# Optimization experiments

Measured on AMD Instinct MI355X. Metric: run time of the kernel, lower is better.

The kernel has to match this reference:

```python
import jax, jax.numpy as jnp
import numpy as np
import math

HEADS = 8
DIM_HEAD = 64


def setup_inputs() -> dict:
    key = jax.random.key(0)
    k1, k2, k3 = jax.random.split(key, 3)
    b, n, dim = 4, 2048, 512
    inner = HEADS * DIM_HEAD  # 512
    x = jax.random.normal(k1, (b, n, dim), dtype=jnp.float32)
    W_qkv = jax.random.normal(k2, (dim, 4 * inner), dtype=jnp.float32) * (dim ** -0.5)
    W_out = jax.random.normal(k3, (2 * inner, dim), dtype=jnp.float32) * ((2 * inner) ** -0.5)
    b_out = jnp.zeros((dim,), dtype=jnp.float32)
    return {"x": x, "W_qkv": W_qkv, "W_out": W_out, "b_out": b_out}


def reference(x, W_qkv, W_out, b_out):
    b, n, d = x.shape
    h, dh = HEADS, DIM_HEAD
    scale = dh ** -0.5
    qkvt = x @ W_qkv  # [b, n, 4*h*dh]
    q, k, v, t = jnp.split(qkvt, 4, axis=-1)
    # 'b n (h d) -> b h n d'
    def to_heads(z):
        return z.reshape(b, n, h, dh).transpose(0, 2, 1, 3)
    q, k, v, t = map(to_heads, (q, k, v, t))

    # Branch 1: standard softmax attention
    dots = jnp.einsum('bhid,bhjd->bhij', q, k) * scale
    attn1 = jax.nn.softmax(dots, axis=-1)
    out1 = jnp.einsum('bhij,bhjd->bhid', attn1, v)

    # Branch 2: fixed positional-decay attention (shared across b, h; no repeat needed)
    pos = jnp.arange(1, n + 1, dtype=x.dtype)  # linspace(1, n, n)
    tg = jnp.abs(pos[None, :] - pos[:, None])  # |j - i|, [n, n]
    attn2 = jnp.exp(-tg / jnp.asarray(math.e, dtype=x.dtype))
    # NOTE: original divides by sum(-1) WITHOUT keepdim -> broadcasts over columns:
    # attn2[i, j] / sum_k attn2[j, k]
    attn2 = attn2 / attn2.sum(-1)
    out2 = jnp.einsum('ij,bhjd->bhid', attn2, t)

    out = jnp.concatenate([out1, out2], axis=-1)  # [b, h, n, 2*dh]
    out = out.transpose(0, 2, 1, 3).reshape(b, n, 2 * h * dh)  # 'b h n d -> b n (h d)'
    return out @ W_out + b_out
```

## Files before the change

kernel.cpp:

```cpp
#include <hip/hip_runtime.h>
#include <hip/hip_bf16.h>

#define B_ 4
#define N_ 2048
#define D_ 512
#define H_ 8
#define DH_ 64

typedef float float4_ __attribute__((ext_vector_type(4)));
typedef int int2_ __attribute__((ext_vector_type(2)));
typedef int int4_ __attribute__((ext_vector_type(4)));
typedef unsigned short ushort4_ __attribute__((ext_vector_type(4)));
typedef unsigned short ushort8_ __attribute__((ext_vector_type(8)));
typedef __bf16 bf16x8 __attribute__((ext_vector_type(8)));
typedef _Float16 half2_ __attribute__((ext_vector_type(2)));
typedef _Float16 half4_ __attribute__((ext_vector_type(4)));
typedef _Float16 half8_ __attribute__((ext_vector_type(8)));

#if __has_builtin(__builtin_amdgcn_exp2f)
#define EXP2(x) __builtin_amdgcn_exp2f(x)
#else
#define EXP2(x) exp2f(x)
#endif

__device__ __forceinline__ float b2f(unsigned short u) {
  union { unsigned int u; float f; } v; v.u = ((unsigned int)u) << 16; return v.f;
}
__device__ __forceinline__ unsigned short f2b(float f) {
  union { float f; unsigned int u; } v; v.f = f;
  unsigned int r = v.u + 0x7fffu + ((v.u >> 16) & 1u);
  return (unsigned short)(r >> 16);
}
__device__ __forceinline__ half4_ pk4(float a, float b, float c, float d) {
  half2_ lo = __builtin_bit_cast(half2_, __builtin_amdgcn_cvt_pkrtz(a, b));
  half2_ hi = __builtin_bit_cast(half2_, __builtin_amdgcn_cvt_pkrtz(c, d));
  return __builtin_bit_cast(half4_,
      (int2_){__builtin_bit_cast(int, lo), __builtin_bit_cast(int, hi)});
}
__device__ __forceinline__ half8_ cat44(half4_ a, half4_ b) {
  int2_ ia = __builtin_bit_cast(int2_, a), ib = __builtin_bit_cast(int2_, b);
  int4_ r = {ia[0], ia[1], ib[0], ib[1]};
  return __builtin_bit_cast(half8_, r);
}

#define GLD16(gp, lp)                                                        \
  __builtin_amdgcn_global_load_lds(                                          \
      (const __attribute__((address_space(1))) unsigned int*)(gp),           \
      (__attribute__((address_space(3))) unsigned int*)(lp), 16, 0, 0)

#define VMCNT(n) asm volatile("s_waitcnt vmcnt(" #n ")" ::: "memory")
#define SCHED0   __builtin_amdgcn_sched_barrier(0)
#define SBAR     __builtin_amdgcn_s_barrier()

__device__ __forceinline__ bool detect_fp32_local(
    const unsigned short* __restrict__ xhdr, int* cnt_sh) {
  if (threadIdx.x == 0) *cnt_sh = 0;
  __syncthreads();
  unsigned int e = (xhdr[threadIdx.x] >> 7) & 0xFFu;
  if (e >= 134u) atomicAdd(cnt_sh, 1);
  __syncthreads();
  return *cnt_sh > 16;
}

__device__ __forceinline__ void transpose_conv(
    const void* __restrict__ src, unsigned short* __restrict__ dst,
    int R, int C, int bx, int by, bool ofp) {
  __shared__ unsigned short tile[32][33];
  const int c0 = bx * 32, r0 = by * 32;
  const int tx = threadIdx.x & 31, ty = threadIdx.x >> 5;
#pragma unroll
  for (int k = 0; k < 4; ++k) {
    int r = ty + k * 8;
    long idx = (long)(r0 + r) * C + c0 + tx;
    tile[r][tx] = ofp ? f2b(((const float*)src)[idx])
                      : ((const unsigned short*)src)[idx];
  }
  __syncthreads();
#pragma unroll
  for (int k = 0; k < 4; ++k) {
    int c = ty + k * 8;
    dst[(long)(c0 + c) * R + r0 + tx] = tile[tx][c];
  }
}

__global__ __launch_bounds__(256) void prep_all(
    const void* __restrict__ xraw, const void* __restrict__ Wqraw,
    const void* __restrict__ Woraw, unsigned short* __restrict__ xb,
    unsigned short* __restrict__ WqT, unsigned short* __restrict__ WoT,
    unsigned short* __restrict__ Wband) {
  __shared__ int cnt_sh;
  const bool ofp = detect_fp32_local((const unsigned short*)xraw, &cnt_sh);
  const int bid = blockIdx.x;
  if (bid < 4096) {
    int i4 = bid * 256 + threadIdx.x;
    ushort4_ o;
    if (ofp) {
      float4_ v = ((const float4_*)xraw)[i4];
      o[0] = f2b(v[0]); o[1] = f2b(v[1]); o[2] = f2b(v[2]); o[3] = f2b(v[3]);
    } else {
      o = ((const ushort4_*)xraw)[i4];
    }
    *(ushort4_*)(xb + (long)i4 * 4) = o;
  } else if (bid < 5120) {
    const int b2 = bid - 4096;
    transpose_conv(Wqraw, WqT, 512, 2048, b2 % 64, b2 / 64, ofp);
  } else if (bid < 5632) {
    const int b2 = bid - 5120;
    transpose_conv(Woraw, WoT, 1024, 512, b2 % 16, b2 / 16, ofp);
  } else {
    constexpr float INV_E = 0.36787944117144233f;
    constexpr float R1 = 0.69220062755534635f;
    constexpr float INV_1MR = 3.2488706f;
    const int i = bid - 5632;
    const int krel = threadIdx.x;
    const int j = (i >> 6) * 64 - 96 + krel;
    float c = 0.f;
    if (j >= 0 && j < N_) {
      float wgt = __expf(-fabsf((float)(i - j)) * INV_E);
      float rj = __expf(-(float)j * INV_E);
      float rnj = __expf(-(float)(N_ - 1 - j) * INV_E);
      float S = 1.f + R1 * (2.f - rj - rnj) * INV_1MR;
      c = wgt / S;
    }
    _Float16 hv = (_Float16)c;
    Wband[i * 256 + krel] = __builtin_bit_cast(unsigned short, hv);
  }
}

#define MFMA16x32(d, a, b) \
  d = __builtin_amdgcn_mfma_f32_16x16x32_bf16(a, b, d, 0, 0, 0)

__global__ __launch_bounds__(512, 2) void gemm256(
    const unsigned short* __restrict__ A, const unsigned short* __restrict__ Bt,
    unsigned short* __restrict__ C, int M, int N, int K) {
  __shared__ unsigned short As[2][16384];
  __shared__ unsigned short Bs[2][16384];
  const int tid = threadIdx.x;
  const int w = tid >> 6, lane = tid & 63, l16 = lane & 15, quad = lane >> 4;
  const int wm = w >> 2, wn = w & 3;
  const int flat = blockIdx.x + blockIdx.y * 32;
  const int xc = flat & 7, jj = flat >> 3;
  const int bx = xc * 4 + (jj & 3), by = jj >> 2;
  const long tm = (long)bx * 256, tn = (long)by * 256;

  const int srow = tid >> 3;
  const int sch = (tid & 7) ^ (srow & 7);
  const unsigned short* gA = A + (tm + srow) * (long)K + sch * 8;
  const unsigned short* gB = Bt + (tn + srow) * (long)K + sch * 8;

  const int xr8 = l16 & 7;
  const int ch0 = ((0 + quad) ^ xr8) * 8;
  const int ch1 = ((4 + quad) ^ xr8) * 8;
  const int rowA0 = (wm * 128 + l16) * 64;
  const int rowB0 = (wn * 64 + l16) * 64;

  float4_ acc[8][4] = {};

  auto stage = [&](int t, int bufn) __attribute__((always_inline)) {
#pragma unroll
    for (int r = 0; r < 4; ++r)
      GLD16(gA + (long)(r * 64) * K + t * 64, &As[bufn][r * 4096 + w * 512]);
#pragma unroll
    for (int r = 0; r < 4; ++r)
      GLD16(gB + (long)(r * 64) * K + t * 64, &Bs[bufn][r * 4096 + w * 512]);
  };

  stage(0, 0);
  asm volatile("s_waitcnt vmcnt(0)" ::: "memory");
  __builtin_amdgcn_s_barrier();

  const int NT = K >> 6;
  for (int t = 0; t < NT; ++t) {
    const int buf = t & 1;
    const unsigned short* as = As[buf];
    const unsigned short* bs = Bs[buf];
    bf16x8 af[8], bq[4], br[4];
#pragma unroll
    for (int mi = 0; mi < 4; ++mi) {
      af[mi * 2]     = __builtin_bit_cast(bf16x8, *(const int4_*)&as[rowA0 + mi * 1024 + ch0]);
      af[mi * 2 + 1] = __builtin_bit_cast(bf16x8, *(const int4_*)&as[rowA0 + mi * 1024 + ch1]);
    }
#pragma unroll
    for (int ni = 0; ni < 2; ++ni) {
      bq[ni * 2]     = __builtin_bit_cast(bf16x8, *(const int4_*)&bs[rowB0 + ni * 1024 + ch0]);
      bq[ni * 2 + 1] = __builtin_bit_cast(bf16x8, *(const int4_*)&bs[rowB0 + ni * 1024 + ch1]);
    }
    if (t + 1 < NT) stage(t + 1, buf ^ 1);
    __builtin_amdgcn_s_barrier();
    asm volatile("s_waitcnt lgkmcnt(0)" ::: "memory");
    __builtin_amdgcn_sched_barrier(0);
    __builtin_amdgcn_s_setprio(1);
#pragma unroll
    for (int mi = 0; mi < 4; ++mi)
#pragma unroll
      for (int ni = 0; ni < 2; ++ni) {
        MFMA16x32(acc[mi][ni], af[mi * 2], bq[ni * 2]);
        MFMA16x32(acc[mi][ni], af[mi * 2 + 1], bq[ni * 2 + 1]);
      }
    __builtin_amdgcn_s_setprio(0);
    __builtin_amdgcn_s_barrier();
#pragma unroll
    for (int ni = 0; ni < 2; ++ni) {
      br[ni * 2]     = __builtin_bit_cast(bf16x8, *(const int4_*)&bs[rowB0 + (2 + ni) * 1024 + ch0]);
      br[ni * 2 + 1] = __builtin_bit_cast(bf16x8, *(const int4_*)&bs[rowB0 + (2 + ni) * 1024 + ch1]);
    }
    __builtin_amdgcn_s_barrier();
    asm volatile("s_waitcnt lgkmcnt(0)" ::: "memory");
    __builtin_amdgcn_sched_barrier(0);
    __builtin_amdgcn_s_setprio(1);
#pragma unroll
    for (int mi = 0; mi < 4; ++mi)
#pragma unroll
      for (int ni = 0; ni < 2; ++ni) {
        MFMA16x32(acc[mi][2 + ni], af[mi * 2], br[ni * 2]);
        MFMA16x32(acc[mi][2 + ni], af[mi * 2 + 1], br[ni * 2 + 1]);
      }
    __builtin_amdgcn_s_setprio(0);
    __builtin_amdgcn_s_barrier();
#pragma unroll
    for (int mi = 0; mi < 4; ++mi) {
      af[mi * 2]     = __builtin_bit_cast(bf16x8, *(const int4_*)&as[rowA0 + (4 + mi) * 1024 + ch0]);
      af[mi * 2 + 1] = __builtin_bit_cast(bf16x8, *(const int4_*)&as[rowA0 + (4 + mi) * 1024 + ch1]);
    }
    __builtin_amdgcn_s_barrier();
    asm volatile("s_waitcnt lgkmcnt(0)" ::: "memory");
    __builtin_amdgcn_sched_barrier(0);
    __builtin_amdgcn_s_setprio(1);
#pragma unroll
    for (int mi = 0; mi < 4; ++mi)
#pragma unroll
      for (int ni = 0; ni < 2; ++ni) {
        MFMA16x32(acc[4 + mi][2 + ni], af[mi * 2], br[ni * 2]);
        MFMA16x32(acc[4 + mi][2 + ni], af[mi * 2 + 1], br[ni * 2 + 1]);
      }
    __builtin_amdgcn_s_setprio(0);
    __builtin_amdgcn_s_barrier();
#pragma unroll
    for (int ni = 0; ni < 2; ++ni) {
      bq[ni * 2]     = __builtin_bit_cast(bf16x8, *(const int4_*)&bs[rowB0 + ni * 1024 + ch0]);
      bq[ni * 2 + 1] = __builtin_bit_cast(bf16x8, *(const int4_*)&bs[rowB0 + ni * 1024 + ch1]);
    }
    __builtin_amdgcn_s_barrier();
    asm volatile("s_waitcnt lgkmcnt(0)" ::: "memory");
    __builtin_amdgcn_sched_barrier(0);
    __builtin_amdgcn_s_setprio(1);
#pragma unroll
    for (int mi = 0; mi < 4; ++mi)
#pragma unroll
      for (int ni = 0; ni < 2; ++ni) {
        MFMA16x32(acc[4 + mi][ni], af[mi * 2], bq[ni * 2]);
        MFMA16x32(acc[4 + mi][ni], af[mi * 2 + 1], bq[ni * 2 + 1]);
      }
    __builtin_amdgcn_s_setprio(0);
    asm volatile("s_waitcnt vmcnt(0)" ::: "memory");
    __builtin_amdgcn_sched_barrier(0);
    __builtin_amdgcn_s_barrier();
  }
#pragma unroll
  for (int ni = 0; ni < 4; ++ni) {
    long col = tn + wn * 64 + ni * 16 + l16;
#pragma unroll
    for (int mi = 0; mi < 8; ++mi)
#pragma unroll
      for (int r = 0; r < 4; ++r) {
        long row = tm + wm * 128 + mi * 16 + quad * 4 + r;
        C[row * N + col] = f2b(acc[mi][ni][r]);
      }
  }
}

__global__ __launch_bounds__(512, 2) void gemm_o(
    const unsigned short* __restrict__ A, const unsigned short* __restrict__ Bt,
    void* __restrict__ C, const void* __restrict__ bias_raw,
    const unsigned short* __restrict__ xhdr) {
  __shared__ int cnt_sh;
  const bool ofp = detect_fp32_local(xhdr, &cnt_sh);
  __shared__ unsigned short As[2][8192];
  __shared__ unsigned short Bs[2][8192];
  constexpr int K = 1024, N = 512;
  const int tid = threadIdx.x;
  const int w = tid >> 6, lane = tid & 63, l16 = lane & 15, quad = lane >> 4;
  const int wm = w >> 2, wn = w & 3;
  const int flat = blockIdx.x + blockIdx.y * 64;
  const int xc = flat & 7, jj = flat >> 3;
  const int bx = xc * 8 + (jj & 7), by = jj >> 3;
  const long tm = (long)bx * 128, tn = (long)by * 128;
  const int srow = tid >> 3;
  const int sch = (tid & 7) ^ (srow & 7);
  const unsigned short* gA = A + (tm + srow) * (long)K + sch * 8;
  const unsigned short* gB = Bt + (tn + srow) * (long)K + sch * 8;
  const int xr8 = l16 & 7;
  const int ch0 = ((0 + quad) ^ xr8) * 8;
  const int ch1 = ((4 + quad) ^ xr8) * 8;
  const int rowA0 = (wm * 64 + l16) * 64;
  const int rowB0 = (wn * 32 + l16) * 64;
  float4_ acc[4][2] = {};

  auto stage = [&](int t, int bufn) __attribute__((always_inline)) {
#pragma unroll
    for (int r = 0; r < 2; ++r)
      GLD16(gA + (long)(r * 64) * K + t * 64, &As[bufn][r * 4096 + w * 512]);
#pragma unroll
    for (int r = 0; r < 2; ++r)
      GLD16(gB + (long)(r * 64) * K + t * 64, &Bs[bufn][r * 4096 + w * 512]);
  };

  stage(0, 0);
  asm volatile("s_waitcnt vmcnt(0)" ::: "memory");
  __builtin_amdgcn_s_barrier();

  const int NT = K >> 6;
  for (int t = 0; t < NT; ++t) {
    const int buf = t & 1;
    const unsigned short* as = As[buf];
    const unsigned short* bs = Bs[buf];
    bf16x8 af[8], bf0[2], bf1[2];
#pragma unroll
    for (int mi = 0; mi < 4; ++mi) {
      af[mi * 2]     = __builtin_bit_cast(bf16x8, *(const int4_*)&as[rowA0 + mi * 1024 + ch0]);
      af[mi * 2 + 1] = __builtin_bit_cast(bf16x8, *(const int4_*)&as[rowA0 + mi * 1024 + ch1]);
    }
    bf0[0] = __builtin_bit_cast(bf16x8, *(const int4_*)&bs[rowB0 + ch0]);
    bf0[1] = __builtin_bit_cast(bf16x8, *(const int4_*)&bs[rowB0 + ch1]);
    if (t + 1 < NT) stage(t + 1, buf ^ 1);
    __builtin_amdgcn_s_barrier();
    asm volatile("s_waitcnt lgkmcnt(0)" ::: "memory");
    __builtin_amdgcn_sched_barrier(0);
    __builtin_amdgcn_s_setprio(1);
#pragma unroll
    for (int mi = 0; mi < 4; ++mi) {
      MFMA16x32(acc[mi][0], af[mi * 2], bf0[0]);
      MFMA16x32(acc[mi][0], af[mi * 2 + 1], bf0[1]);
    }
    __builtin_amdgcn_s_setprio(0);
    __builtin_amdgcn_s_barrier();
    bf1[0] = __builtin_bit_cast(bf16x8, *(const int4_*)&bs[rowB0 + 1024 + ch0]);
    bf1[1] = __builtin_bit_cast(bf16x8, *(const int4_*)&bs[rowB0 + 1024 + ch1]);
    __builtin_amdgcn_s_barrier();
    asm volatile("s_waitcnt lgkmcnt(0)" ::: "memory");
    __builtin_amdgcn_sched_barrier(0);
    __builtin_amdgcn_s_setprio(1);
#pragma unroll
    for (int mi = 0; mi < 4; ++mi) {
      MFMA16x32(acc[mi][1], af[mi * 2], bf1[0]);
      MFMA16x32(acc[mi][1], af[mi * 2 + 1], bf1[1]);
    }
    __builtin_amdgcn_s_setprio(0);
    asm volatile("s_waitcnt vmcnt(0)" ::: "memory");
    __builtin_amdgcn_sched_barrier(0);
    __builtin_amdgcn_s_barrier();
  }
#pragma unroll
  for (int nb = 0; nb < 2; ++nb) {
    long col = tn + wn * 32 + nb * 16 + l16;
    float bv = ofp ? ((const float*)bias_raw)[col]
                   : b2f(((const unsigned short*)bias_raw)[col]);
#pragma unroll
    for (int mb = 0; mb < 4; ++mb)
#pragma unroll
      for (int r = 0; r < 4; ++r) {
        long row = tm + wm * 64 + mb * 16 + quad * 4 + r;
        float val = acc[mb][nb][r] + bv;
        if (ofp) ((float*)C)[row * N + col] = val;
        else ((unsigned short*)C)[row * N + col] = f2b(val);
      }
  }
}

#define TSW 266
__global__ __launch_bounds__(256) void mid_all(
    const unsigned short* __restrict__ qkvt, unsigned short* __restrict__ Vt,
    const unsigned short* __restrict__ Wband, unsigned short* __restrict__ catb) {
  __shared__ __align__(16) unsigned short Ts[64 * TSW];
  const int bid = blockIdx.x;
  const int tid = threadIdx.x;
  if (bid < 512) {
    unsigned int* Td = (unsigned int*)Ts;
    const int bh = bid >> 4, b = bh >> 3, h = bh & 7;
    const int j0 = (bid & 15) * 128;
    const int dg = tid & 7;
#pragma unroll
    for (int it = 0; it < 2; ++it) {
      const int jp = (tid >> 3) + 32 * it;
      const long base =
          (long)(b * N_ + j0 + 2 * jp) * 2048 + 1024 + h * 64 + dg * 8;
      ushort8_ r0 = __builtin_bit_cast(ushort8_, *(const int4_*)&qkvt[base]);
      ushort8_ r1 = __builtin_bit_cast(ushort8_, *(const int4_*)&qkvt[base + 2048]);
#pragma unroll
      for (int e = 0; e < 8; ++e) {
        const int d = dg * 8 + e;
        const int S = (d >> 3) | ((d & 1) << 3);
        unsigned short h0 = __builtin_bit_cast(unsigned short, (_Float16)b2f(r0[e]));
        unsigned short h1 = __builtin_bit_cast(unsigned short, (_Float16)b2f(r1[e]));
        Td[d * 68 + (jp ^ (S << 2))] = (unsigned int)h0 | ((unsigned int)h1 << 16);
      }
    }
    __syncthreads();
#pragma unroll
    for (int it = 0; it < 4; ++it) {
      const int d = (tid >> 4) + 16 * it;
      const int ch = tid & 15;
      const int S = (d >> 3) | ((d & 1) << 3);
      int4_ v = *(const int4_*)&Td[d * 68 + ((ch ^ S) << 2)];
      *(int4_*)&Vt[((long)bh * 64 + d) * 2048 + j0 + ch * 8] = v;
    }
    return;
  }
  const int b2 = bid - 512;
  const int qtile = b2 & 31;
  const int bh = b2 >> 5, b = bh >> 3, h = bh & 7;
  const int jlo = qtile * 64 - 96;
  {
    unsigned int* Tsd = (unsigned int*)Ts;
    const int dg = tid & 7;
#pragma unroll
    for (int it = 0; it < 4; ++it) {
      const int kkp = (tid >> 3) + 32 * it;
      const int jA = jlo + 2 * kkp, jB = jA + 1;
      int4_ r0 = {}, r1 = {};
      if (jA >= 0 && jA < N_)
        r0 = *(const int4_*)&qkvt[(long)(b * N_ + jA) * 2048 + 1536 + h * 64 + dg * 8];
      if (jB >= 0 && jB < N_)
        r1 = *(const int4_*)&qkvt[(long)(b * N_ + jB) * 2048 + 1536 + h * 64 + dg * 8];
      ushort8_ u0 = __builtin_bit_cast(ushort8_, r0);
      ushort8_ u1 = __builtin_bit_cast(ushort8_, r1);
#pragma unroll
      for (int e = 0; e < 8; ++e) {
        const int d = dg * 8 + e;
        unsigned short h0 = __builtin_bit_cast(unsigned short, (_Float16)b2f(u0[e]));
        unsigned short h1 = __builtin_bit_cast(unsigned short, (_Float16)b2f(u1[e]));
        Tsd[d * 133 + kkp] = (unsigned int)h0 | ((unsigned int)h1 << 16);
      }
    }
  }
  __syncthreads();
  const int w = tid >> 6, lane = tid & 63, l16 = lane & 15, quad = lane >> 4;
  const int i_row = qtile * 64 + w * 16 + l16;
  const unsigned short* ap = Wband + i_row * 256;
  float4_ acc[4] = {};
#pragma unroll
  for (int kh = 0; kh < 8; ++kh) {
    half8_ af = __builtin_bit_cast(half8_, *(const int4_*)&ap[kh * 32 + quad * 8]);
#pragma unroll
    for (int nb = 0; nb < 4; ++nb) {
      half8_ bf = __builtin_bit_cast(half8_,
          *(const int4_*)&Ts[(nb * 16 + l16) * TSW + kh * 32 + quad * 8]);
      acc[nb] = __builtin_amdgcn_mfma_f32_16x16x32_f16(af, bf, acc[nb], 0, 0, 0);
    }
  }
#pragma unroll
  for (int nb = 0; nb < 4; ++nb)
#pragma unroll
    for (int r = 0; r < 4; ++r) {
      int row = qtile * 64 + w * 16 + quad * 4 + r;
      catb[(long)(b * N_ + row) * 1024 + h * 128 + 64 + nb * 16 + l16] =
          f2b(acc[nb][r]);
    }
}

__global__ __launch_bounds__(256) void flash_kernel(
    const unsigned short* __restrict__ qkvt, const unsigned short* __restrict__ Vt,
    unsigned short* __restrict__ catb) {
  __shared__ unsigned short Ks[4][64 * 64];
  __shared__ unsigned short Vs[4][64 * 64];
  const int flat = blockIdx.x + blockIdx.y * 16;
  const int slot = flat & 7, idx = flat >> 3;
  const int bh = slot * 4 + (idx >> 4);
  const int i0 = (idx & 15) * 128;
  const int b = bh >> 3, h = bh & 7;
  const int tid = threadIdx.x;
  const int w = tid >> 6, lane = tid & 63, l16 = lane & 15, quad = lane >> 4;
  const int srow8 = lane >> 3, sch = lane & 7;
  const int chK = sch ^ srow8;
  bf16x8 qf[2][2];
  {
    constexpr float SCL = 0.125f * 1.44269504088896f;
#pragma unroll
    for (int s2 = 0; s2 < 2; ++s2) {
      const long qrow =
          (long)(b * N_ + i0 + w * 32 + s2 * 16 + l16) * 2048 + h * 64;
#pragma unroll
      for (int kh = 0; kh < 2; ++kh) {
        ushort8_ raw = __builtin_bit_cast(ushort8_,
            *(const int4_*)&qkvt[qrow + kh * 32 + quad * 8]);
        ushort8_ sc;
#pragma unroll
        for (int e = 0; e < 8; ++e) sc[e] = f2b(b2f(raw[e]) * SCL);
        qf[s2][kh] = __builtin_bit_cast(bf16x8, sc);
      }
    }
  }
  const unsigned short* kp[2];
#pragma unroll
  for (int kh = 0; kh < 2; ++kh)
    kp[kh] = &Ks[0][l16 * 64 + (((kh * 4 + quad) ^ (l16 & 7)) * 8)];
  const unsigned short* vp32[2];
#pragma unroll
  for (int wd = 0; wd < 2; ++wd)
    vp32[wd] = &Vs[0][l16 * 64 + (((wd * 4 + quad) ^ (l16 & 7)) * 8)];
  const unsigned short* kg[2];
  const unsigned short* vg[2];
#pragma unroll
  for (int g = 0; g < 2; ++g) {
    const int prow = w * 16 + g * 8 + srow8;
    const int ptok = (prow & 0x20) | ((prow & 0x10) >> 2) |
                     ((prow & 0x0C) << 1) | (prow & 3);
    kg[g] = qkvt + (long)(b * N_ + ptok) * 2048 + 512 + h * 64 + chK * 8;
    vg[g] = Vt + ((long)bh * 64 + prow) * 2048 + chK * 8;
  }
  float4_ O[2][4] = {};
  float4_ O5[2] = {};
  const half8_ ones8 = {(_Float16)1.f, (_Float16)1.f, (_Float16)1.f, (_Float16)1.f,
                        (_Float16)1.f, (_Float16)1.f, (_Float16)1.f, (_Float16)1.f};

  auto stage_k = [&](int jt_, int buf_) __attribute__((always_inline)) {
    const int j0 = jt_ * 64;
#pragma unroll
    for (int g = 0; g < 2; ++g)
      GLD16(kg[g] + (long)j0 * 2048,
            (char*)&Ks[0][0] + buf_ * 8192 + (w * 16 + g * 8) * 128);
  };
  auto stage_v = [&](int jt_, int buf_) __attribute__((always_inline)) {
    const int j0 = jt_ * 64;
#pragma unroll
    for (int g = 0; g < 2; ++g)
      GLD16(vg[g] + j0,
            (char*)&Vs[0][0] + buf_ * 8192 + (w * 16 + g * 8) * 128);
  };
  auto pv_step = [&](half4_ (&pf)[2][4], int vb) __attribute__((always_inline)) {
#pragma unroll
    for (int wd = 0; wd < 2; ++wd) {
      half8_ pa0 = cat44(pf[0][2 * wd], pf[0][2 * wd + 1]);
      half8_ pa1 = cat44(pf[1][2 * wd], pf[1][2 * wd + 1]);
#pragma unroll
      for (int dblk = 0; dblk < 4; ++dblk) {
        half8_ vfv = *(const half8_*)(vp32[wd] + vb + dblk * 1024);
        O[0][dblk] = __builtin_amdgcn_mfma_f32_16x16x32_f16(
            pa0, vfv, O[0][dblk], 0, 0, 0);
        O[1][dblk] = __builtin_amdgcn_mfma_f32_16x16x32_f16(
            pa1, vfv, O[1][dblk], 0, 0, 0);
      }
      O5[0] = __builtin_amdgcn_mfma_f32_16x16x32_f16(pa0, ones8, O5[0], 0, 0, 0);
      O5[1] = __builtin_amdgcn_mfma_f32_16x16x32_f16(pa1, ones8, O5[1], 0, 0, 0);
    }
  };
  auto phase_body = [&](int i, half4_ (&pfp)[2][4], half4_ (&pfc)[2][4],
                        bool first, bool stK, bool stV)
      __attribute__((always_inline)) {
    if (stK) stage_k(i + 2, (i + 2) & 3);
    if (stV) stage_v(i + 1, (i + 1) & 3);
    const int kb = (i & 3) * 4096;
    float4_ s[2][4] = {};
#pragma unroll
    for (int kh = 0; kh < 2; ++kh)
#pragma unroll
      for (int c = 0; c < 4; ++c) {
        bf16x8 kf = __builtin_bit_cast(bf16x8,
            *(const int4_*)(kp[kh] + kb + c * 1024));
#pragma unroll
        for (int s2 = 0; s2 < 2; ++s2)
          s[s2][c] = __builtin_amdgcn_mfma_f32_16x16x32_bf16(
              kf, qf[s2][kh], s[s2][c], 0, 0, 0);
      }
    if (!first) pv_step(pfp, ((i - 1) & 3) * 4096);
#pragma unroll
    for (int s2 = 0; s2 < 2; ++s2)
#pragma unroll
      for (int c = 0; c < 4; ++c)
        pfc[s2][c] = pk4(EXP2(s[s2][c][0]), EXP2(s[s2][c][1]),
                         EXP2(s[s2][c][2]), EXP2(s[s2][c][3]));
  };

  half4_ pfA[2][4], pfB[2][4];
  stage_k(0, 0);
  stage_k(1, 1);
  stage_v(0, 0);
  VMCNT(4); SCHED0; SBAR;
  phase_body(0, pfB, pfA, true, true, true);
  VMCNT(4); SCHED0; SBAR;
  for (int jt = 1; jt < 29; jt += 2) {
    phase_body(jt, pfA, pfB, false, true, true);
    VMCNT(4); SCHED0; SBAR;
    phase_body(jt + 1, pfB, pfA, false, true, true);
    VMCNT(4); SCHED0; SBAR;
  }
  phase_body(29, pfA, pfB, false, true, true);
  VMCNT(4); SCHED0; SBAR;
  phase_body(30, pfB, pfA, false, false, true);
  VMCNT(2); SCHED0; SBAR;
  phase_body(31, pfA, pfB, false, false, false);
  VMCNT(0); SCHED0; SBAR;
  pv_step(pfB, (31 & 3) * 4096);

#pragma unroll
  for (int s2 = 0; s2 < 2; ++s2) {
    float linv[4];
#pragma unroll
    for (int r = 0; r < 4; ++r) linv[r] = 1.f / O5[s2][r];
#pragma unroll
    for (int dblk = 0; dblk < 4; ++dblk)
#pragma unroll
      for (int r = 0; r < 4; ++r) {
        int row = i0 + w * 32 + s2 * 16 + quad * 4 + r;
        catb[(long)(b * N_ + row) * 1024 + h * 128 + dblk * 16 + l16] =
            f2b(O[s2][dblk][r] * linv[r]);
      }
  }
}

extern "C" void kernel_launch(void* const* d_in, const int* in_sizes, int n_in,
                              void* d_out, int out_size, void* d_ws, size_t ws_size,
                              hipStream_t stream) {
  char* ws = (char*)d_ws;
  unsigned short* qkvt = (unsigned short*)(ws);
  unsigned short* WqT  = (unsigned short*)(ws + (size_t)32 * 1024 * 1024);
  unsigned short* WoT  = (unsigned short*)(ws + (size_t)34 * 1024 * 1024);
  unsigned short* Vt   = (unsigned short*)(ws + (size_t)35 * 1024 * 1024);
  unsigned short* catb = (unsigned short*)(ws + (size_t)43 * 1024 * 1024);
  unsigned short* xb   = (unsigned short*)(ws + (size_t)59 * 1024 * 1024);
  unsigned short* Wband= (unsigned short*)(ws + (size_t)68 * 1024 * 1024);

  prep_all<<<7680, 256, 0, stream>>>(d_in[0], d_in[1], d_in[2],
                                     xb, WqT, WoT, Wband);
  gemm256<<<dim3(8192 / 256, 2048 / 256), 512, 0, stream>>>(
      xb, WqT, qkvt, 8192, 2048, 512);
  mid_all<<<1536, 256, 0, stream>>>(qkvt, Vt, Wband, catb);
  flash_kernel<<<dim3(2048 / 128, 32), 256, 0, stream>>>(qkvt, Vt, catb);
  gemm_o<<<dim3(8192 / 128, 512 / 128), 512, 0, stream>>>(
      catb, WoT, d_out, d_in[3], (const unsigned short*)d_in[0]);
}
```

Before: 182.8 us.

## Split V transpose into own kernel and fuse band attention into flash launch

The V-transpose pass becomes its own small kernel, and the positional-decay band matmul blocks now run inside the same launch as the flash attention blocks, indexed by block id. The aim is to fill the GPU tail of the flash kernel with the independent band work and to remove a serialized launch boundary between them. The cost is a larger shared-memory footprint (64KB) for the band blocks, which may lower their occupancy, and block scheduling order now decides how well the two kinds of work overlap.

```diff
diff --git a/kernel.cpp b/kernel.cpp
--- a/kernel.cpp
+++ b/kernel.cpp
@@ -367,108 +367,109 @@
   }
 }
 
-#define TSW 266
-__global__ __launch_bounds__(256) void mid_all(
-    const unsigned short* __restrict__ qkvt, unsigned short* __restrict__ Vt,
-    const unsigned short* __restrict__ Wband, unsigned short* __restrict__ catb) {
-  __shared__ __align__(16) unsigned short Ts[64 * TSW];
+__global__ __launch_bounds__(256) void vt_only(
+    const unsigned short* __restrict__ qkvt, unsigned short* __restrict__ Vt) {
+  __shared__ __align__(16) unsigned int Td[64 * 68];
   const int bid = blockIdx.x;
   const int tid = threadIdx.x;
-  if (bid < 512) {
-    unsigned int* Td = (unsigned int*)Ts;
-    const int bh = bid >> 4, b = bh >> 3, h = bh & 7;
-    const int j0 = (bid & 15) * 128;
-    const int dg = tid & 7;
-#pragma unroll
-    for (int it = 0; it < 2; ++it) {
-      const int jp = (tid >> 3) + 32 * it;
-      const long base =
-          (long)(b * N_ + j0 + 2 * jp) * 2048 + 1024 + h * 64 + dg * 8;
-      ushort8_ r0 = __builtin_bit_cast(ushort8_, *(const int4_*)&qkvt[base]);
-      ushort8_ r1 = __builtin_bit_cast(ushort8_, *(const int4_*)&qkvt[base + 2048]);
-#pragma unroll
-      for (int e = 0; e < 8; ++e) {
-        const int d = dg * 8 + e;
-        const int S = (d >> 3) | ((d & 1) << 3);
-        unsigned short h0 = __builtin_bit_cast(unsigned short, (_Float16)b2f(r0[e]));
-        unsigned short h1 = __builtin_bit_cast(unsigned short, (_Float16)b2f(r1[e]));
-        Td[d * 68 + (jp ^ (S << 2))] = (unsigned int)h0 | ((unsigned int)h1 << 16);
+  const int bh = bid >> 4, b = bh >> 3, h = bh & 7;
+  const int j0 = (bid & 15) * 128;
+  const int dg = tid & 7;
+#pragma unroll
+  for (int it = 0; it < 2; ++it) {
+    const int jp = (tid >> 3) + 32 * it;
+    const long base =
+        (long)(b * N_ + j0 + 2 * jp) * 2048 + 1024 + h * 64 + dg * 8;
+    ushort8_ r0 = __builtin_bit_cast(ushort8_, *(const int4_*)&qkvt[base]);
+    ushort8_ r1 = __builtin_bit_cast(ushort8_, *(const int4_*)&qkvt[base + 2048]);
+#pragma unroll
+    for (int e = 0; e < 8; ++e) {
+      const int d = dg * 8 + e;
+      const int S = (d >> 3) | ((d & 1) << 3);
+      unsigned short h0 = __builtin_bit_cast(unsigned short, (_Float16)b2f(r0[e]));
+      unsigned short h1 = __builtin_bit_cast(unsigned short, (_Float16)b2f(r1[e]));
+      Td[d * 68 + (jp ^ (S << 2))] = (unsigned int)h0 | ((unsigned int)h1 << 16);
+    }
+  }
+  __syncthreads();
+#pragma unroll
+  for (int it = 0; it < 4; ++it) {
+    const int d = (tid >> 4) + 16 * it;
+    const int ch = tid & 15;
+    const int S = (d >> 3) | ((d & 1) << 3);
+    int4_ v = *(const int4_*)&Td[d * 68 + ((ch ^ S) << 2)];
+    *(int4_*)&Vt[((long)bh * 64 + d) * 2048 + j0 + ch * 8] = v;
+  }
+}
+
+#define TSW 266
+__global__ __launch_bounds__(256) void flash_mid(
+    const unsigned short* __restrict__ qkvt, const unsigned short* __restrict__ Vt,
+    const unsigned short* __restrict__ Wband, unsigned short* __restrict__ catb) {
+  __shared__ __align__(16) unsigned short shm[32768];
+  const int bid = blockIdx.x;
+  const int tid = threadIdx.x;
+  if (bid < 1024) {
+    unsigned short* Ts = shm;
+    const int b2 = bid;
+    const int qtile = b2 & 31;
+    const int bh = b2 >> 5, b = bh >> 3, h = bh & 7;
+    const int jlo = qtile * 64 - 96;
+    {
+      unsigned int* Tsd = (unsigned int*)Ts;
+      const int dg = tid & 7;
+#pragma unroll
+      for (int it = 0; it < 4; ++it) {
+        const int kkp = (tid >> 3) + 32 * it;
+        const int jA = jlo + 2 * kkp, jB = jA + 1;
+        int4_ r0 = {}, r1 = {};
+        if (jA >= 0 && jA < N_)
+          r0 = *(const int4_*)&qkvt[(long)(b * N_ + jA) * 2048 + 1536 + h * 64 + dg * 8];
+        if (jB >= 0 && jB < N_)
+          r1 = *(const int4_*)&qkvt[(long)(b * N_ + jB) * 2048 + 1536 + h * 64 + dg * 8];
+        ushort8_ u0 = __builtin_bit_cast(ushort8_, r0);
+        ushort8_ u1 = __builtin_bit_cast(ushort8_, r1);
+#pragma unroll
+        for (int e = 0; e < 8; ++e) {
+          const int d = dg * 8 + e;
+          unsigned short h0 = __builtin_bit_cast(unsigned short, (_Float16)b2f(u0[e]));
+          unsigned short h1 = __builtin_bit_cast(unsigned short, (_Float16)b2f(u1[e]));
+          Tsd[d * 133 + kkp] = (unsigned int)h0 | ((unsigned int)h1 << 16);
+        }
       }
     }
     __syncthreads();
-#pragma unroll
-    for (int it = 0; it < 4; ++it) {
-      const int d = (tid >> 4) + 16 * it;
-      const int ch = tid & 15;
-      const int S = (d >> 3) | ((d & 1) << 3);
-      int4_ v = *(const int4_*)&Td[d * 68 + ((ch ^ S) << 2)];
-      *(int4_*)&Vt[((long)bh * 64 + d) * 2048 + j0 + ch * 8] = v;
-    }
+    const int w = tid >> 6, lane = tid & 63, l16 = lane & 15, quad = lane >> 4;
+    const int i_row = qtile * 64 + w * 16 + l16;
+    const unsigned short* ap = Wband + i_row * 256;
+    float4_ acc[4] = {};
+#pragma unroll
+    for (int kh = 0; kh < 8; ++kh) {
+      half8_ af = __builtin_bit_cast(half8_, *(const int4_*)&ap[kh * 32 + quad * 8]);
+#pragma unroll
+      for (int nb = 0; nb < 4; ++nb) {
+        half8_ bf = __builtin_bit_cast(half8_,
+            *(const int4_*)&Ts[(nb * 16 + l16) * TSW + kh * 32 + quad * 8]);
+        acc[nb] = __builtin_amdgcn_mfma_f32_16x16x32_f16(af, bf, acc[nb], 0, 0, 0);
+      }
+    }
+#pragma unroll
+    for (int nb = 0; nb < 4; ++nb)
+#pragma unroll
+      for (int r = 0; r < 4; ++r) {
+        int row = qtile * 64 + w * 16 + quad * 4 + r;
+        catb[(long)(b * N_ + row) * 1024 + h * 128 + 64 + nb * 16 + l16] =
+            f2b(acc[nb][r]);
+      }
     return;
   }
-  const int b2 = bid - 512;
-  const int qtile = b2 & 31;
-  const int bh = b2 >> 5, b = bh >> 3, h = bh & 7;
-  const int jlo = qtile * 64 - 96;
-  {
-    unsigned int* Tsd = (unsigned int*)Ts;
-    const int dg = tid & 7;
-#pragma unroll
-    for (int it = 0; it < 4; ++it) {
-      const int kkp = (tid >> 3) + 32 * it;
-      const int jA = jlo + 2 * kkp, jB = jA + 1;
-      int4_ r0 = {}, r1 = {};
-      if (jA >= 0 && jA < N_)
-        r0 = *(const int4_*)&qkvt[(long)(b * N_ + jA) * 2048 + 1536 + h * 64 + dg * 8];
-      if (jB >= 0 && jB < N_)
-        r1 = *(const int4_*)&qkvt[(long)(b * N_ + jB) * 2048 + 1536 + h * 64 + dg * 8];
-      ushort8_ u0 = __builtin_bit_cast(ushort8_, r0);
-      ushort8_ u1 = __builtin_bit_cast(ushort8_, r1);
-#pragma unroll
-      for (int e = 0; e < 8; ++e) {
-        const int d = dg * 8 + e;
-        unsigned short h0 = __builtin_bit_cast(unsigned short, (_Float16)b2f(u0[e]));
-        unsigned short h1 = __builtin_bit_cast(unsigned short, (_Float16)b2f(u1[e]));
-        Tsd[d * 133 + kkp] = (unsigned int)h0 | ((unsigned int)h1 << 16);
-      }
-    }
-  }
-  __syncthreads();
-  const int w = tid >> 6, lane = tid & 63, l16 = lane & 15, quad = lane >> 4;
-  const int i_row = qtile * 64 + w * 16 + l16;
-  const unsigned short* ap = Wband + i_row * 256;
-  float4_ acc[4] = {};
-#pragma unroll
-  for (int kh = 0; kh < 8; ++kh) {
-    half8_ af = __builtin_bit_cast(half8_, *(const int4_*)&ap[kh * 32 + quad * 8]);
-#pragma unroll
-    for (int nb = 0; nb < 4; ++nb) {
-      half8_ bf = __builtin_bit_cast(half8_,
-          *(const int4_*)&Ts[(nb * 16 + l16) * TSW + kh * 32 + quad * 8]);
-      acc[nb] = __builtin_amdgcn_mfma_f32_16x16x32_f16(af, bf, acc[nb], 0, 0, 0);
-    }
-  }
-#pragma unroll
-  for (int nb = 0; nb < 4; ++nb)
-#pragma unroll
-    for (int r = 0; r < 4; ++r) {
-      int row = qtile * 64 + w * 16 + quad * 4 + r;
-      catb[(long)(b * N_ + row) * 1024 + h * 128 + 64 + nb * 16 + l16] =
-          f2b(acc[nb][r]);
-    }
-}
-
-__global__ __launch_bounds__(256) void flash_kernel(
-    const unsigned short* __restrict__ qkvt, const unsigned short* __restrict__ Vt,
-    unsigned short* __restrict__ catb) {
-  __shared__ unsigned short Ks[4][64 * 64];
-  __shared__ unsigned short Vs[4][64 * 64];
-  const int flat = blockIdx.x + blockIdx.y * 16;
+  unsigned short* KsB = shm;
+  unsigned short* VsB = shm + 16384;
+  const int flat = bid - 1024;
   const int slot = flat & 7, idx = flat >> 3;
   const int bh = slot * 4 + (idx >> 4);
   const int i0 = (idx & 15) * 128;
   const int b = bh >> 3, h = bh & 7;
-  const int tid = threadIdx.x;
   const int w = tid >> 6, lane = tid & 63, l16 = lane & 15, quad = lane >> 4;
   const int srow8 = lane >> 3, sch = lane & 7;
   const int chK = sch ^ srow8;
@@ -493,11 +494,11 @@
   const unsigned short* kp[2];
 #pragma unroll
   for (int kh = 0; kh < 2; ++kh)
-    kp[kh] = &Ks[0][l16 * 64 + (((kh * 4 + quad) ^ (l16 & 7)) * 8)];
+    kp[kh] = KsB + l16 * 64 + (((kh * 4 + quad) ^ (l16 & 7)) * 8);
   const unsigned short* vp32[2];
 #pragma unroll
   for (int wd = 0; wd < 2; ++wd)
-    vp32[wd] = &Vs[0][l16 * 64 + (((wd * 4 + quad) ^ (l16 & 7)) * 8)];
+    vp32[wd] = VsB + l16 * 64 + (((wd * 4 + quad) ^ (l16 & 7)) * 8);
   const unsigned short* kg[2];
   const unsigned short* vg[2];
 #pragma unroll
@@ -518,14 +519,14 @@
 #pragma unroll
     for (int g = 0; g < 2; ++g)
       GLD16(kg[g] + (long)j0 * 2048,
-            (char*)&Ks[0][0] + buf_ * 8192 + (w * 16 + g * 8) * 128);
+            (char*)KsB + buf_ * 8192 + (w * 16 + g * 8) * 128);
   };
   auto stage_v = [&](int jt_, int buf_) __attribute__((always_inline)) {
     const int j0 = jt_ * 64;
 #pragma unroll
     for (int g = 0; g < 2; ++g)
       GLD16(vg[g] + j0,
-            (char*)&Vs[0][0] + buf_ * 8192 + (w * 16 + g * 8) * 128);
+            (char*)VsB + buf_ * 8192 + (w * 16 + g * 8) * 128);
   };
   auto pv_step = [&](half4_ (&pf)[2][4], int vb) __attribute__((always_inline)) {
 #pragma unroll
@@ -624,8 +625,8 @@
                                      xb, WqT, WoT, Wband);
   gemm256<<<dim3(8192 / 256, 2048 / 256), 512, 0, stream>>>(
       xb, WqT, qkvt, 8192, 2048, 512);
-  mid_all<<<1536, 256, 0, stream>>>(qkvt, Vt, Wband, catb);
-  flash_kernel<<<dim3(2048 / 128, 32), 256, 0, stream>>>(qkvt, Vt, catb);
+  vt_only<<<512, 256, 0, stream>>>(qkvt, Vt);
+  flash_mid<<<1536, 256, 0, stream>>>(qkvt, Vt, Wband, catb);
   gemm_o<<<dim3(8192 / 128, 512 / 128), 512, 0, stream>>>(
       catb, WoT, d_out, d_in[3], (const unsigned short*)d_in[0]);
 }
```

Result: no change. 185.3 us (+1.4%).

## Fuse V transpose into QKV GEMM epilogue, drop transpose blocks from mid kernel

Applied to the files above, without the earlier changes.

The QKV GEMM epilogue now also writes the V columns (tiles by==4,5) directly into the transposed fp16 Vt layout, so the separate 512-block transpose phase in the mid kernel is removed and mid2 only runs the decay-band part. This avoids re-reading V from global memory and one pass of LDS transposition. In exchange the GEMM epilogue for those tiles issues extra 8-byte strided stores, which are less coalesced than the previous transpose's 16-byte writes.

```diff
diff --git a/kernel.cpp b/kernel.cpp
--- a/kernel.cpp
+++ b/kernel.cpp
@@ -132,7 +132,8 @@
 
 __global__ __launch_bounds__(512, 2) void gemm256(
     const unsigned short* __restrict__ A, const unsigned short* __restrict__ Bt,
-    unsigned short* __restrict__ C, int M, int N, int K) {
+    unsigned short* __restrict__ C, unsigned short* __restrict__ Vt,
+    int M, int N, int K) {
   __shared__ unsigned short As[2][16384];
   __shared__ unsigned short Bs[2][16384];
   const int tid = threadIdx.x;
@@ -266,6 +267,26 @@
         long row = tm + wm * 128 + mi * 16 + quad * 4 + r;
         C[row * N + col] = f2b(acc[mi][ni][r]);
       }
+  }
+  if (by == 4 || by == 5) {
+    const int bb = (int)(tm >> 11);
+    const int tok0 = ((int)tm & 2047) + wm * 128;
+#pragma unroll
+    for (int ni = 0; ni < 4; ++ni) {
+      const int cv = (int)(tn + wn * 64 + ni * 16 + l16) - 1024;
+      const int h = cv >> 6, d = cv & 63;
+      unsigned short* vrow = Vt + ((long)(bb * 8 + h) * 64 + d) * 2048;
+#pragma unroll
+      for (int mi = 0; mi < 8; ++mi) {
+        ushort4_ o;
+#pragma unroll
+        for (int r = 0; r < 4; ++r) {
+          _Float16 hv = (_Float16)b2f(f2b(acc[mi][ni][r]));
+          o[r] = __builtin_bit_cast(unsigned short, hv);
+        }
+        *(ushort4_*)&vrow[tok0 + mi * 16 + quad * 4] = o;
+      }
+    }
   }
 }
 
@@ -368,47 +389,14 @@
 }
 
 #define TSW 266
-__global__ __launch_bounds__(256) void mid_all(
-    const unsigned short* __restrict__ qkvt, unsigned short* __restrict__ Vt,
+__global__ __launch_bounds__(256) void mid2(
+    const unsigned short* __restrict__ qkvt,
     const unsigned short* __restrict__ Wband, unsigned short* __restrict__ catb) {
   __shared__ __align__(16) unsigned short Ts[64 * TSW];
   const int bid = blockIdx.x;
   const int tid = threadIdx.x;
-  if (bid < 512) {
-    unsigned int* Td = (unsigned int*)Ts;
-    const int bh = bid >> 4, b = bh >> 3, h = bh & 7;
-    const int j0 = (bid & 15) * 128;
-    const int dg = tid & 7;
-#pragma unroll
-    for (int it = 0; it < 2; ++it) {
-      const int jp = (tid >> 3) + 32 * it;
-      const long base =
-          (long)(b * N_ + j0 + 2 * jp) * 2048 + 1024 + h * 64 + dg * 8;
-      ushort8_ r0 = __builtin_bit_cast(ushort8_, *(const int4_*)&qkvt[base]);
-      ushort8_ r1 = __builtin_bit_cast(ushort8_, *(const int4_*)&qkvt[base + 2048]);
-#pragma unroll
-      for (int e = 0; e < 8; ++e) {
-        const int d = dg * 8 + e;
-        const int S = (d >> 3) | ((d & 1) << 3);
-        unsigned short h0 = __builtin_bit_cast(unsigned short, (_Float16)b2f(r0[e]));
-        unsigned short h1 = __builtin_bit_cast(unsigned short, (_Float16)b2f(r1[e]));
-        Td[d * 68 + (jp ^ (S << 2))] = (unsigned int)h0 | ((unsigned int)h1 << 16);
-      }
-    }
-    __syncthreads();
-#pragma unroll
-    for (int it = 0; it < 4; ++it) {
-      const int d = (tid >> 4) + 16 * it;
-      const int ch = tid & 15;
-      const int S = (d >> 3) | ((d & 1) << 3);
-      int4_ v = *(const int4_*)&Td[d * 68 + ((ch ^ S) << 2)];
-      *(int4_*)&Vt[((long)bh * 64 + d) * 2048 + j0 + ch * 8] = v;
-    }
-    return;
-  }
-  const int b2 = bid - 512;
-  const int qtile = b2 & 31;
-  const int bh = b2 >> 5, b = bh >> 3, h = bh & 7;
+  const int qtile = bid & 31;
+  const int bh = bid >> 5, b = bh >> 3, h = bh & 7;
   const int jlo = qtile * 64 - 96;
   {
     unsigned int* Tsd = (unsigned int*)Ts;
@@ -623,8 +611,8 @@
   prep_all<<<7680, 256, 0, stream>>>(d_in[0], d_in[1], d_in[2],
                                      xb, WqT, WoT, Wband);
   gemm256<<<dim3(8192 / 256, 2048 / 256), 512, 0, stream>>>(
-      xb, WqT, qkvt, 8192, 2048, 512);
-  mid_all<<<1536, 256, 0, stream>>>(qkvt, Vt, Wband, catb);
+      xb, WqT, qkvt, Vt, 8192, 2048, 512);
+  mid2<<<1024, 256, 0, stream>>>(qkvt, Wband, catb);
   flash_kernel<<<dim3(2048 / 128, 32), 256, 0, stream>>>(qkvt, Vt, catb);
   gemm_o<<<dim3(8192 / 128, 512 / 128), 512, 0, stream>>>(
       catb, WoT, d_out, d_in[3], (const unsigned short*)d_in[0]);
```

After: 186.4 us. +2.0%, slower.
